# Kernel optimization log

Hardware: AMD Instinct MI355X
Metric: run time of the kernel (lower is better)

Reference implementation:

```python
import jax, jax.numpy as jnp
import numpy as np

MAX_BITS = 64
HID = 768
B = 32768


def setup_inputs() -> dict:
    key = jax.random.key(0)
    ks = jax.random.split(key, 16)
    s = 0.02

    def w(k, shape):
        return jax.random.normal(k, shape, jnp.float32) * s

    a_bits = jnp.round(jax.random.uniform(ks[0], (B, MAX_BITS))).astype(jnp.float32)
    shift_amount = jax.random.randint(ks[1], (B,), 0, MAX_BITS).astype(jnp.int32)
    return {
        "a_bits": a_bits,
        "shift_amount": shift_amount,
        # shift_decoder: 64 -> 768 -> 768 -> 64 (weights stored [in, out])
        "Ws0": w(ks[2], (MAX_BITS, HID)), "bs0": jnp.zeros((HID,), jnp.float32),
        "Ws1": w(ks[3], (HID, HID)),      "bs1": jnp.zeros((HID,), jnp.float32),
        "Ws2": w(ks[4], (HID, MAX_BITS)), "bs2": jnp.zeros((MAX_BITS,), jnp.float32),
        # index_net: 128 -> 768 -> 768 -> 64
        "Wi0": w(ks[5], (2 * MAX_BITS, HID)), "bi0": jnp.zeros((HID,), jnp.float32),
        "Wi1": w(ks[6], (HID, HID)),          "bi1": jnp.zeros((HID,), jnp.float32),
        "Wi2": w(ks[7], (HID, MAX_BITS)),     "bi2": jnp.zeros((MAX_BITS,), jnp.float32),
        # validity_net: 128 -> 384 -> 1
        "Wv0": w(ks[8], (2 * MAX_BITS, HID // 2)), "bv0": jnp.zeros((HID // 2,), jnp.float32),
        "Wv1": w(ks[9], (HID // 2, 1)),            "bv1": jnp.zeros((1,), jnp.float32),
    }


def reference(a_bits, shift_amount, Ws0, bs0, Ws1, bs1, Ws2, bs2,
              Wi0, bi0, Wi1, bi1, Wi2, bi2, Wv0, bv0, Wv1, bv1):
    bits = a_bits.shape[1]  # == MAX_BITS == 64
    # decompose integer shift into bits: [B, bits]
    shift_bits = ((shift_amount[:, None] >> jnp.arange(bits, dtype=shift_amount.dtype)) & 1).astype(jnp.float32)
    # shift_decoder MLP -> hard one-hot of predicted shift
    h = jax.nn.relu(shift_bits @ Ws0 + bs0)
    h = jax.nn.relu(h @ Ws1 + bs1)
    shift_logits = (h @ Ws2 + bs2)[:, :bits]
    shift_soft = jax.nn.one_hot(jnp.argmax(shift_logits, axis=-1), bits, dtype=jnp.float32)  # [B, bits]
    # combined = [out_pos(one_hot(i)), shift_soft]; out_pos contribution to layer-0 is just row i of the
    # first `bits` rows of the weight, so precompute the shift_soft part once.
    base_i = shift_soft @ Wi0[bits:] + bi0   # [B, HID]
    base_v = shift_soft @ Wv0[bits:] + bv0   # [B, HID//2]

    def step(carry, i):
        h1 = jax.nn.relu(base_i + Wi0[i])                 # [B, HID]
        h2 = jax.nn.relu(h1 @ Wi1 + bi1)                  # [B, HID]
        idx_logits = (h2 @ Wi2 + bi2)[:, :bits]           # [B, bits]
        idx_soft = jax.nn.one_hot(jnp.argmax(idx_logits, axis=-1), bits, dtype=jnp.float32)
        pointed = jnp.sum(idx_soft * a_bits, axis=1)      # [B] soft gather
        hv = jax.nn.relu(base_v + Wv0[i])                 # [B, HID//2]
        valid = (hv @ Wv1 + bv1)[:, 0]                    # [B]
        return carry, pointed * jax.nn.sigmoid(valid)

    _, outs = jax.lax.scan(step, None, jnp.arange(bits))  # [bits, B]
    return outs.T                                          # [B, bits]
```

## Files before the change

### kernel.cpp

```cpp
#include <hip/hip_runtime.h>
#include <math.h>

#define HID 768
#define NB  64
#define HV  384

__device__ __forceinline__ float4 ld4(const float* p) { return *(const float4*)p; }

__global__ __launch_bounds__(256)
void dec1p_kernel(const float* __restrict__ Ws0, const float* __restrict__ bs0,
                  const float* __restrict__ Ws1, float* __restrict__ H1p) {
    __shared__ float W0s[7 * 48];
    __shared__ float As[48 * 68];
    __shared__ float Bs[48 * 36];
    const int tid = threadIdx.x;
    const int n0 = (blockIdx.x % 24) * 32;
    const int kz = blockIdx.x / 24;
    const int ks = kz * 48;

    for (int e = tid; e < 7 * 48; e += 256) {
        const int r = e / 48, c = e % 48;
        W0s[e] = (r < 6) ? Ws0[(size_t)r * HID + ks + c] : bs0[ks + c];
    }
    for (int e = tid; e < 48 * 8; e += 256) {
        const int k = e >> 3, nq = (e & 7) * 4;
        *(float4*)&Bs[k * 36 + nq] = ld4(Ws1 + (size_t)(ks + k) * HID + n0 + nq);
    }
    __syncthreads();
    for (int e = tid; e < 48 * 64; e += 256) {
        const int k = e >> 6, t = e & 63;
        float v = W0s[6 * 48 + k];
        #pragma unroll
        for (int b = 0; b < 6; ++b)
            v = fmaf((float)((t >> b) & 1), W0s[b * 48 + k], v);
        As[k * 68 + t] = fmaxf(v, 0.f);
    }
    __syncthreads();

    const int tx = tid & 7, ty = tid >> 3;
    float acc[2][4] = {};
    #pragma unroll 8
    for (int kk = 0; kk < 48; ++kk) {
        const float2 a2 = *(const float2*)&As[kk * 68 + ty * 2];
        const float4 b4 = *(const float4*)&Bs[kk * 36 + tx * 4];
        const float av[2] = {a2.x, a2.y};
        const float bv[4] = {b4.x, b4.y, b4.z, b4.w};
        #pragma unroll
        for (int a = 0; a < 2; ++a)
            #pragma unroll
            for (int b = 0; b < 4; ++b)
                acc[a][b] = fmaf(av[a], bv[b], acc[a][b]);
    }
    #pragma unroll
    for (int a = 0; a < 2; ++a) {
        float4 o = make_float4(acc[a][0], acc[a][1], acc[a][2], acc[a][3]);
        *(float4*)&H1p[((size_t)kz * 64 + ty * 2 + a) * HID + n0 + tx * 4] = o;
    }
}

__global__ __launch_bounds__(256)
void dec2_kernel(const float* __restrict__ H1p, const float* __restrict__ bs1,
                 const float* __restrict__ Ws2, const float* __restrict__ bs2,
                 int* __restrict__ pred) {
    __shared__ float sh[HID];
    __shared__ float plp[4][64];
    const int tid = threadIdx.x;
    const int t = blockIdx.x;

    for (int e = tid; e < HID / 4; e += 256) {
        const int k4 = e * 4;
        float4 v = ld4(bs1 + k4);
        #pragma unroll
        for (int z = 0; z < 16; ++z) {
            const float4 p = ld4(H1p + ((size_t)z * 64 + t) * HID + k4);
            v.x += p.x; v.y += p.y; v.z += p.z; v.w += p.w;
        }
        sh[k4 + 0] = fmaxf(v.x, 0.f);
        sh[k4 + 1] = fmaxf(v.y, 0.f);
        sh[k4 + 2] = fmaxf(v.z, 0.f);
        sh[k4 + 3] = fmaxf(v.w, 0.f);
    }
    __syncthreads();
    {
        const int n = tid & 63, part = tid >> 6;
        float p = 0.f;
        #pragma unroll 8
        for (int kk = 0; kk < 192; ++kk) {
            const int k = part * 192 + kk;
            p = fmaf(sh[k], Ws2[k * 64 + n], p);
        }
        plp[part][n] = p;
    }
    __syncthreads();
    if (tid == 0) {
        int best = 0;
        float bv = bs2[0] + plp[0][0] + plp[1][0] + plp[2][0] + plp[3][0];
        for (int n = 1; n < 64; ++n) {
            const float x = bs2[n] + plp[0][n] + plp[1][n] + plp[2][n] + plp[3][n];
            if (x > bv) { bv = x; best = n; }
        }
        pred[t] = best;
    }
}

__global__ __launch_bounds__(64)
void plan_kernel(const int* __restrict__ pred, int* __restrict__ hdr) {
    const int lane = threadIdx.x;
    __shared__ int present[64];
    present[lane] = 0;
    __syncthreads();
    present[pred[lane] & 63] = 1;
    __syncthreads();
    const unsigned long long alive = __ballot(present[lane] != 0);
    const int P = __popcll(alive);
    const int rank = __popcll(alive & ((1ull << lane) - 1ull));
    if (lane == 0) hdr[0] = P;
    if (present[lane]) { hdr[1 + rank] = lane; hdr[65 + lane] = rank; }
    else hdr[65 + lane] = -1;
}

__global__ __launch_bounds__(256)
void gemmA_kernel(const float* __restrict__ Wi0, const float* __restrict__ bi0,
                  const float* __restrict__ Wi1, const int* __restrict__ hdr,
                  float* __restrict__ H2p) {
    __shared__ float As[64 * 68];
    __shared__ float Bs[64 * 68];
    const int tid = threadIdx.x;
    const int P = hdr[0];
    const int li = blockIdx.y;
    if (li >= P) return;
    const int s = hdr[1 + li];
    const int n0 = blockIdx.x * 64;
    const int z = blockIdx.z;
    const int tx = tid & 15, ty = tid >> 4;
    const float* arow = Wi0 + (size_t)(64 + s) * HID;
    float acc[4][4] = {};

    for (int kt = 0; kt < 2; ++kt) {
        const int k0 = z * 128 + kt * 64;
        #pragma unroll
        for (int pass = 0; pass < 4; ++pass) {
            const int c = pass * 256 + tid;
            const int m = c >> 4, kq = (c & 15) * 4;
            const float4 a1 = ld4(arow + k0 + kq);
            const float4 a2 = ld4(Wi0 + (size_t)m * HID + k0 + kq);
            const float4 bb = ld4(bi0 + k0 + kq);
            As[(kq + 0) * 68 + m] = fmaxf(a1.x + a2.x + bb.x, 0.f);
            As[(kq + 1) * 68 + m] = fmaxf(a1.y + a2.y + bb.y, 0.f);
            As[(kq + 2) * 68 + m] = fmaxf(a1.z + a2.z + bb.z, 0.f);
            As[(kq + 3) * 68 + m] = fmaxf(a1.w + a2.w + bb.w, 0.f);
        }
        #pragma unroll
        for (int pass = 0; pass < 4; ++pass) {
            const int c = pass * 256 + tid;
            const int k = c >> 4, nq = (c & 15) * 4;
            *(float4*)&Bs[k * 68 + nq] = ld4(Wi1 + (size_t)(k0 + k) * HID + n0 + nq);
        }
        __syncthreads();
        #pragma unroll 8
        for (int kk = 0; kk < 64; ++kk) {
            const float4 a4 = *(const float4*)&As[kk * 68 + ty * 4];
            const float4 b4 = *(const float4*)&Bs[kk * 68 + tx * 4];
            const float av[4] = {a4.x, a4.y, a4.z, a4.w};
            const float bv[4] = {b4.x, b4.y, b4.z, b4.w};
            #pragma unroll
            for (int a = 0; a < 4; ++a)
                #pragma unroll
                for (int b = 0; b < 4; ++b)
                    acc[a][b] = fmaf(av[a], bv[b], acc[a][b]);
        }
        __syncthreads();
    }
    float* dst = H2p + ((size_t)(z * 64 + li) * 64) * HID + n0;
    #pragma unroll
    for (int a = 0; a < 4; ++a) {
        float4 o = make_float4(acc[a][0], acc[a][1], acc[a][2], acc[a][3]);
        *(float4*)(dst + (size_t)(ty * 4 + a) * HID + tx * 4) = o;
    }
}

__global__ __launch_bounds__(256)
void gemmB_kernel(const float* __restrict__ bi1, const float* __restrict__ Wi2,
                  const int* __restrict__ hdr, const float* __restrict__ H2p,
                  float* __restrict__ PLf) {
    __shared__ float Ht[64 * 68];
    __shared__ float W2[64 * 68];
    const int tid = threadIdx.x;
    const int P = hdr[0];
    const int li = blockIdx.y;
    if (li >= P) return;
    const int bx = blockIdx.x;
    const int n0 = bx * 64;
    const size_t zstep = (size_t)64 * 64 * HID;

    for (int e = tid; e < 1024; e += 256) {
        const int m = e >> 4, nq = (e & 15) * 4;
        const float* base = H2p + ((size_t)li * 64 + m) * HID + n0 + nq;
        float4 v = ld4(base);
        #pragma unroll
        for (int z = 1; z < 6; ++z) {
            const float4 p = ld4(base + z * zstep);
            v.x += p.x; v.y += p.y; v.z += p.z; v.w += p.w;
        }
        const float4 bb = ld4(bi1 + n0 + nq);
        Ht[(nq + 0) * 68 + m] = fmaxf(v.x + bb.x, 0.f);
        Ht[(nq + 1) * 68 + m] = fmaxf(v.y + bb.y, 0.f);
        Ht[(nq + 2) * 68 + m] = fmaxf(v.z + bb.z, 0.f);
        Ht[(nq + 3) * 68 + m] = fmaxf(v.w + bb.w, 0.f);
    }
    #pragma unroll
    for (int pass = 0; pass < 4; ++pass) {
        const int c = pass * 256 + tid;
        const int cl = c >> 4, oq = (c & 15) * 4;
        *(float4*)&W2[cl * 68 + oq] = ld4(Wi2 + (size_t)(n0 + cl) * 64 + oq);
    }
    __syncthreads();
    const int tx = tid & 15, ty = tid >> 4;
    float pl_[4][4] = {};
    #pragma unroll 16
    for (int kk = 0; kk < 64; ++kk) {
        const float4 a4 = *(const float4*)&Ht[kk * 68 + ty * 4];
        const float4 b4 = *(const float4*)&W2[kk * 68 + tx * 4];
        const float av[4] = {a4.x, a4.y, a4.z, a4.w};
        const float bv[4] = {b4.x, b4.y, b4.z, b4.w};
        #pragma unroll
        for (int a = 0; a < 4; ++a)
            #pragma unroll
            for (int b = 0; b < 4; ++b)
                pl_[a][b] = fmaf(av[a], bv[b], pl_[a][b]);
    }
    #pragma unroll
    for (int a = 0; a < 4; ++a) {
        float4 o = make_float4(pl_[a][0], pl_[a][1], pl_[a][2], pl_[a][3]);
        *(float4*)&PLf[((size_t)(bx * 64 + li) * 64 + ty * 4 + a) * 64 + tx * 4] = o;
    }
}

__global__ __launch_bounds__(256)
void reduceA_kernel(const float* __restrict__ PLf, const float* __restrict__ bi2,
                    const float* __restrict__ Wv0, const float* __restrict__ bv0,
                    const float* __restrict__ Wv1, const float* __restrict__ bv1,
                    const int* __restrict__ hdr,
                    int* __restrict__ j_tab, float* __restrict__ sig_tab) {
    __shared__ float lg[16 * 68];
    const int tid = threadIdx.x;
    const int s = blockIdx.x >> 2;
    const int li = hdr[65 + s];
    if (li < 0) return;
    const int r0 = blockIdx.x * 16;
    const int rr = tid >> 4, q = tid & 15;
    const int i = (r0 & 63) + rr;
    float4 v = ld4(bi2 + q * 4);
    #pragma unroll
    for (int bx = 0; bx < 12; ++bx) {
        const float4 p = ld4(PLf + ((size_t)(bx * 64 + li) * 64 + i) * 64 + q * 4);
        v.x += p.x; v.y += p.y; v.z += p.z; v.w += p.w;
    }
    *(float4*)&lg[rr * 68 + q * 4] = v;
    __syncthreads();
    if (tid < 16) {
        int best = 0; float bv = lg[tid * 68];
        for (int n = 1; n < 64; ++n) {
            const float x = lg[tid * 68 + n];
            if (x > bv) { bv = x; best = n; }
        }
        j_tab[r0 + tid] = best;
    }
    {
        const int r = r0 + rr;
        const int ii = r & 63;
        const float* w1 = Wv0 + (size_t)(64 + s) * HV;
        const float* w2 = Wv0 + (size_t)ii * HV;
        float sum = 0.f;
        #pragma unroll 4
        for (int c = q; c < HV; c += 16) {
            const float hv = fmaxf(w1[c] + w2[c] + bv0[c], 0.f);
            sum = fmaf(hv, Wv1[c], sum);
        }
        #pragma unroll
        for (int m = 8; m >= 1; m >>= 1) sum += __shfl_xor(sum, m);
        if (q == 0) sig_tab[r] = 1.f / (1.f + expf(-(sum + bv1[0])));
    }
}

__global__ __launch_bounds__(256)
void output_kernel(const float* __restrict__ a_bits, const int* __restrict__ shift_amount,
                   const int* __restrict__ pred, const int* __restrict__ j_tab,
                   const float* __restrict__ sig_tab, float* __restrict__ out, int B) {
    const int tid = threadIdx.x;
    const int i = tid & 63;
    const int b = blockIdx.x * 4 + (tid >> 6);
    if (b >= B) return;
    const int t = shift_amount[b] & 63;
    const int s = pred[t];
    const int idx = s * 64 + i;
    const int j = j_tab[idx];
    out[(size_t)b * 64 + i] = a_bits[(size_t)b * 64 + j] * sig_tab[idx];
}

extern "C" void kernel_launch(void* const* d_in, const int* in_sizes, int n_in,
                              void* d_out, int out_size, void* d_ws, size_t ws_size,
                              hipStream_t stream) {
    const float* a_bits       = (const float*)d_in[0];
    const int*   shift_amount = (const int*)d_in[1];
    const float* Ws0 = (const float*)d_in[2];
    const float* bs0 = (const float*)d_in[3];
    const float* Ws1 = (const float*)d_in[4];
    const float* bs1 = (const float*)d_in[5];
    const float* Ws2 = (const float*)d_in[6];
    const float* bs2 = (const float*)d_in[7];
    const float* Wi0 = (const float*)d_in[8];
    const float* bi0 = (const float*)d_in[9];
    const float* Wi1 = (const float*)d_in[10];
    const float* bi1 = (const float*)d_in[11];
    const float* Wi2 = (const float*)d_in[12];
    const float* bi2 = (const float*)d_in[13];
    const float* Wv0 = (const float*)d_in[14];
    const float* bv0 = (const float*)d_in[15];
    const float* Wv1 = (const float*)d_in[16];
    const float* bv1 = (const float*)d_in[17];
    float* out = (float*)d_out;
    const int B = in_sizes[1];

    char* ws = (char*)d_ws;
    int*   pred    = (int*)ws;
    int*   j_tab   = (int*)(ws + 1024);
    float* sig_tab = (float*)(ws + 20480);
    int*   hdr     = (int*)(ws + 40960);
    float* H1p = (float*)(ws + 65536);
    float* H2p = (float*)(ws + 65536);
    float* PLf = (float*)(ws + 65536 + 75497472);

    dec1p_kernel<<<384, 256, 0, stream>>>(Ws0, bs0, Ws1, H1p);
    dec2_kernel<<<64, 256, 0, stream>>>(H1p, bs1, Ws2, bs2, pred);
    plan_kernel<<<1, 64, 0, stream>>>(pred, hdr);
    gemmA_kernel<<<dim3(12, 64, 6), 256, 0, stream>>>(Wi0, bi0, Wi1, hdr, H2p);
    gemmB_kernel<<<dim3(12, 64), 256, 0, stream>>>(bi1, Wi2, hdr, H2p, PLf);
    reduceA_kernel<<<256, 256, 0, stream>>>(PLf, bi2, Wv0, bv0, Wv1, bv1, hdr,
                                            j_tab, sig_tab);
    output_kernel<<<(B + 3) / 4, 256, 0, stream>>>(a_bits, shift_amount, pred,
                                                   j_tab, sig_tab, out, B);
}
```

Before: 153.9 us.

## Fuse plan and reduce kernels into predecessors via atomic last-block tickets

Removes two kernel launches. plan_kernel now runs inside dec2 through a last-block-done atomic ticket. reduceA now runs inside gemmB, where the last 256 ticketed blocks spin until all 768 blocks finish and then do the reduction. This saves launch gaps between small dependent kernels. The cost is a spin-wait that relies on every block being resident or already finished, plus extra threadfences.

```diff
diff --git a/kernel.cpp b/kernel.cpp
--- a/kernel.cpp
+++ b/kernel.cpp
@@ -9,11 +9,13 @@
 
 __global__ __launch_bounds__(256)
 void dec1p_kernel(const float* __restrict__ Ws0, const float* __restrict__ bs0,
-                  const float* __restrict__ Ws1, float* __restrict__ H1p) {
+                  const float* __restrict__ Ws1, float* __restrict__ H1p,
+                  int* __restrict__ cnt) {
     __shared__ float W0s[7 * 48];
     __shared__ float As[48 * 68];
     __shared__ float Bs[48 * 36];
     const int tid = threadIdx.x;
+    if (blockIdx.x == 0 && tid == 0) { cnt[0] = 0; cnt[1] = 0; }
     const int n0 = (blockIdx.x % 24) * 32;
     const int kz = blockIdx.x / 24;
     const int ks = kz * 48;
@@ -61,9 +63,11 @@
 __global__ __launch_bounds__(256)
 void dec2_kernel(const float* __restrict__ H1p, const float* __restrict__ bs1,
                  const float* __restrict__ Ws2, const float* __restrict__ bs2,
-                 int* __restrict__ pred) {
+                 int* __restrict__ pred, int* __restrict__ hdr,
+                 int* __restrict__ cnt) {
     __shared__ float sh[HID];
     __shared__ float plp[4][64];
+    __shared__ int sh_tk;
     const int tid = threadIdx.x;
     const int t = blockIdx.x;
 
@@ -101,22 +105,26 @@
         }
         pred[t] = best;
     }
-}
-
-__global__ __launch_bounds__(64)
-void plan_kernel(const int* __restrict__ pred, int* __restrict__ hdr) {
-    const int lane = threadIdx.x;
-    __shared__ int present[64];
-    present[lane] = 0;
-    __syncthreads();
-    present[pred[lane] & 63] = 1;
-    __syncthreads();
-    const unsigned long long alive = __ballot(present[lane] != 0);
-    const int P = __popcll(alive);
-    const int rank = __popcll(alive & ((1ull << lane) - 1ull));
-    if (lane == 0) hdr[0] = P;
-    if (present[lane]) { hdr[1 + rank] = lane; hdr[65 + lane] = rank; }
-    else hdr[65 + lane] = -1;
+    __threadfence();
+    __syncthreads();
+    if (tid == 0) sh_tk = atomicAdd(&cnt[0], 1);
+    __syncthreads();
+    if (sh_tk == 63) {
+        __threadfence();
+        __shared__ int present[64];
+        if (tid < 64) present[tid] = 0;
+        __syncthreads();
+        if (tid < 64) present[pred[tid] & 63] = 1;
+        __syncthreads();
+        if (tid < 64) {
+            const unsigned long long alive = __ballot(present[tid] != 0);
+            const int P = __popcll(alive);
+            const int rank = __popcll(alive & ((1ull << tid) - 1ull));
+            if (tid == 0) hdr[0] = P;
+            if (present[tid]) { hdr[1 + rank] = tid; hdr[65 + tid] = rank; }
+            else hdr[65 + tid] = -1;
+        }
+    }
 }
 
 __global__ __launch_bounds__(256)
@@ -180,80 +188,94 @@
 }
 
 __global__ __launch_bounds__(256)
-void gemmB_kernel(const float* __restrict__ bi1, const float* __restrict__ Wi2,
-                  const int* __restrict__ hdr, const float* __restrict__ H2p,
-                  float* __restrict__ PLf) {
+void gemmBR_kernel(const float* __restrict__ bi1, const float* __restrict__ Wi2,
+                   const int* __restrict__ hdr, const float* __restrict__ H2p,
+                   float* __restrict__ PLf,
+                   const float* __restrict__ bi2,
+                   const float* __restrict__ Wv0, const float* __restrict__ bv0,
+                   const float* __restrict__ Wv1, const float* __restrict__ bv1,
+                   int* __restrict__ j_tab, float* __restrict__ sig_tab,
+                   int* __restrict__ cnt) {
     __shared__ float Ht[64 * 68];
     __shared__ float W2[64 * 68];
+    __shared__ int sh_tk;
     const int tid = threadIdx.x;
     const int P = hdr[0];
     const int li = blockIdx.y;
-    if (li >= P) return;
     const int bx = blockIdx.x;
     const int n0 = bx * 64;
     const size_t zstep = (size_t)64 * 64 * HID;
 
-    for (int e = tid; e < 1024; e += 256) {
-        const int m = e >> 4, nq = (e & 15) * 4;
-        const float* base = H2p + ((size_t)li * 64 + m) * HID + n0 + nq;
-        float4 v = ld4(base);
-        #pragma unroll
-        for (int z = 1; z < 6; ++z) {
-            const float4 p = ld4(base + z * zstep);
-            v.x += p.x; v.y += p.y; v.z += p.z; v.w += p.w;
-        }
-        const float4 bb = ld4(bi1 + n0 + nq);
-        Ht[(nq + 0) * 68 + m] = fmaxf(v.x + bb.x, 0.f);
-        Ht[(nq + 1) * 68 + m] = fmaxf(v.y + bb.y, 0.f);
-        Ht[(nq + 2) * 68 + m] = fmaxf(v.z + bb.z, 0.f);
-        Ht[(nq + 3) * 68 + m] = fmaxf(v.w + bb.w, 0.f);
-    }
-    #pragma unroll
-    for (int pass = 0; pass < 4; ++pass) {
-        const int c = pass * 256 + tid;
-        const int cl = c >> 4, oq = (c & 15) * 4;
-        *(float4*)&W2[cl * 68 + oq] = ld4(Wi2 + (size_t)(n0 + cl) * 64 + oq);
-    }
-    __syncthreads();
-    const int tx = tid & 15, ty = tid >> 4;
-    float pl_[4][4] = {};
-    #pragma unroll 16
-    for (int kk = 0; kk < 64; ++kk) {
-        const float4 a4 = *(const float4*)&Ht[kk * 68 + ty * 4];
-        const float4 b4 = *(const float4*)&W2[kk * 68 + tx * 4];
-        const float av[4] = {a4.x, a4.y, a4.z, a4.w};
-        const float bv[4] = {b4.x, b4.y, b4.z, b4.w};
-        #pragma unroll
-        for (int a = 0; a < 4; ++a)
+    if (li < P) {
+        for (int e = tid; e < 1024; e += 256) {
+            const int m = e >> 4, nq = (e & 15) * 4;
+            const float* base = H2p + ((size_t)li * 64 + m) * HID + n0 + nq;
+            float4 v = ld4(base);
             #pragma unroll
-            for (int b = 0; b < 4; ++b)
-                pl_[a][b] = fmaf(av[a], bv[b], pl_[a][b]);
-    }
-    #pragma unroll
-    for (int a = 0; a < 4; ++a) {
-        float4 o = make_float4(pl_[a][0], pl_[a][1], pl_[a][2], pl_[a][3]);
-        *(float4*)&PLf[((size_t)(bx * 64 + li) * 64 + ty * 4 + a) * 64 + tx * 4] = o;
-    }
-}
-
-__global__ __launch_bounds__(256)
-void reduceA_kernel(const float* __restrict__ PLf, const float* __restrict__ bi2,
-                    const float* __restrict__ Wv0, const float* __restrict__ bv0,
-                    const float* __restrict__ Wv1, const float* __restrict__ bv1,
-                    const int* __restrict__ hdr,
-                    int* __restrict__ j_tab, float* __restrict__ sig_tab) {
-    __shared__ float lg[16 * 68];
-    const int tid = threadIdx.x;
-    const int s = blockIdx.x >> 2;
-    const int li = hdr[65 + s];
-    if (li < 0) return;
-    const int r0 = blockIdx.x * 16;
+            for (int z = 1; z < 6; ++z) {
+                const float4 p = ld4(base + z * zstep);
+                v.x += p.x; v.y += p.y; v.z += p.z; v.w += p.w;
+            }
+            const float4 bb = ld4(bi1 + n0 + nq);
+            Ht[(nq + 0) * 68 + m] = fmaxf(v.x + bb.x, 0.f);
+            Ht[(nq + 1) * 68 + m] = fmaxf(v.y + bb.y, 0.f);
+            Ht[(nq + 2) * 68 + m] = fmaxf(v.z + bb.z, 0.f);
+            Ht[(nq + 3) * 68 + m] = fmaxf(v.w + bb.w, 0.f);
+        }
+        #pragma unroll
+        for (int pass = 0; pass < 4; ++pass) {
+            const int c = pass * 256 + tid;
+            const int cl = c >> 4, oq = (c & 15) * 4;
+            *(float4*)&W2[cl * 68 + oq] = ld4(Wi2 + (size_t)(n0 + cl) * 64 + oq);
+        }
+        __syncthreads();
+        const int tx = tid & 15, ty = tid >> 4;
+        float pl_[4][4] = {};
+        #pragma unroll 16
+        for (int kk = 0; kk < 64; ++kk) {
+            const float4 a4 = *(const float4*)&Ht[kk * 68 + ty * 4];
+            const float4 b4 = *(const float4*)&W2[kk * 68 + tx * 4];
+            const float av[4] = {a4.x, a4.y, a4.z, a4.w};
+            const float bv[4] = {b4.x, b4.y, b4.z, b4.w};
+            #pragma unroll
+            for (int a = 0; a < 4; ++a)
+                #pragma unroll
+                for (int b = 0; b < 4; ++b)
+                    pl_[a][b] = fmaf(av[a], bv[b], pl_[a][b]);
+        }
+        #pragma unroll
+        for (int a = 0; a < 4; ++a) {
+            float4 o = make_float4(pl_[a][0], pl_[a][1], pl_[a][2], pl_[a][3]);
+            *(float4*)&PLf[((size_t)(bx * 64 + li) * 64 + ty * 4 + a) * 64 + tx * 4] = o;
+        }
+    }
+
+    __threadfence();
+    __syncthreads();
+    if (tid == 0) sh_tk = atomicAdd(&cnt[1], 1);
+    __syncthreads();
+    const int tk = sh_tk;
+    if (tk < 512) return;
+    const int r = tk - 512;
+    const int s = r >> 2;
+    const int li2 = hdr[65 + s];
+    if (li2 < 0) return;
+    if (tid == 0) {
+        while (__hip_atomic_load(&cnt[1], __ATOMIC_RELAXED, __HIP_MEMORY_SCOPE_AGENT) < 768) {
+            __builtin_amdgcn_s_sleep(8);
+        }
+    }
+    __syncthreads();
+    __threadfence();
+
+    float* lg = Ht;
+    const int r0 = r * 16;
     const int rr = tid >> 4, q = tid & 15;
     const int i = (r0 & 63) + rr;
     float4 v = ld4(bi2 + q * 4);
     #pragma unroll
-    for (int bx = 0; bx < 12; ++bx) {
-        const float4 p = ld4(PLf + ((size_t)(bx * 64 + li) * 64 + i) * 64 + q * 4);
+    for (int bx2 = 0; bx2 < 12; ++bx2) {
+        const float4 p = ld4(PLf + ((size_t)(bx2 * 64 + li2) * 64 + i) * 64 + q * 4);
         v.x += p.x; v.y += p.y; v.z += p.z; v.w += p.w;
     }
     *(float4*)&lg[rr * 68 + q * 4] = v;
@@ -267,8 +289,8 @@
         j_tab[r0 + tid] = best;
     }
     {
-        const int r = r0 + rr;
-        const int ii = r & 63;
+        const int rrow = r0 + rr;
+        const int ii = rrow & 63;
         const float* w1 = Wv0 + (size_t)(64 + s) * HV;
         const float* w2 = Wv0 + (size_t)ii * HV;
         float sum = 0.f;
@@ -279,7 +301,7 @@
         }
         #pragma unroll
         for (int m = 8; m >= 1; m >>= 1) sum += __shfl_xor(sum, m);
-        if (q == 0) sig_tab[r] = 1.f / (1.f + expf(-(sum + bv1[0])));
+        if (q == 0) sig_tab[rrow] = 1.f / (1.f + expf(-(sum + bv1[0])));
     }
 }
 
@@ -327,17 +349,17 @@
     int*   j_tab   = (int*)(ws + 1024);
     float* sig_tab = (float*)(ws + 20480);
     int*   hdr     = (int*)(ws + 40960);
+    int*   cnt     = (int*)(ws + 49152);
     float* H1p = (float*)(ws + 65536);
     float* H2p = (float*)(ws + 65536);
     float* PLf = (float*)(ws + 65536 + 75497472);
 
-    dec1p_kernel<<<384, 256, 0, stream>>>(Ws0, bs0, Ws1, H1p);
-    dec2_kernel<<<64, 256, 0, stream>>>(H1p, bs1, Ws2, bs2, pred);
-    plan_kernel<<<1, 64, 0, stream>>>(pred, hdr);
+    dec1p_kernel<<<384, 256, 0, stream>>>(Ws0, bs0, Ws1, H1p, cnt);
+    dec2_kernel<<<64, 256, 0, stream>>>(H1p, bs1, Ws2, bs2, pred, hdr, cnt);
     gemmA_kernel<<<dim3(12, 64, 6), 256, 0, stream>>>(Wi0, bi0, Wi1, hdr, H2p);
-    gemmB_kernel<<<dim3(12, 64), 256, 0, stream>>>(bi1, Wi2, hdr, H2p, PLf);
-    reduceA_kernel<<<256, 256, 0, stream>>>(PLf, bi2, Wv0, bv0, Wv1, bv1, hdr,
-                                            j_tab, sig_tab);
+    gemmBR_kernel<<<dim3(12, 64), 256, 0, stream>>>(bi1, Wi2, hdr, H2p, PLf,
+                                                    bi2, Wv0, bv0, Wv1, bv1,
+                                                    j_tab, sig_tab, cnt);
     output_kernel<<<(B + 3) / 4, 256, 0, stream>>>(a_bits, shift_amount, pred,
                                                    j_tab, sig_tab, out, B);
 }
```

Result: slower. 219.2 us (+42.4%).
